# Kernel tuning notes

Hardware: AMD Instinct MI355X
Metric: run time of the kernel (lower is better)

Reference implementation:

```python
import jax, jax.numpy as jnp
import numpy as np
from jax import lax

SHAPE = (128, 128, 32)
N = 150000
DN = ('NDHWC', 'DHWIO', 'NDHWC')

W_SPECS = [(3, 3, 32), (3, 32, 32), (3, 32, 64), (3, 64, 64), (3, 64, 64),
           (3, 64, 96), (3, 96, 96), (2, 96, 96), (3, 96, 128), (3, 128, 128),
           (3, 128, 160), (3, 160, 160), (3, 160, 192), (3, 192, 192),
           (3, 192, 224), (3, 224, 224), (2, 224, 128), (2, 128, 64)]


def _conv(x, w, s, p):
    return lax.conv_general_dilated(x, w, (s, s, s), p, dimension_numbers=DN)


def _subm(x, w, m):
    # submanifold conv: inactive inputs are exactly 0, outputs masked to active sites
    return _conv(x, w, 1, 'SAME') * m


def _mask_pool(m, k, s, p):
    return lax.reduce_window(m, 0., lax.max, (1, k, k, k, 1), (1, s, s, s, 1), p)


def _max_pool(x, m):
    # sparse max-pool: max over ACTIVE sites only; inactive -> -inf, empty windows -> 0
    xi = jnp.where(m > 0, x, -jnp.inf)
    p = lax.reduce_window(xi, -jnp.inf, lax.max, (1, 2, 2, 2, 1), (1, 2, 2, 2, 1), 'VALID')
    mn = _mask_pool(m, 2, 2, 'VALID')
    return jnp.where(mn > 0, p, 0.), mn


def setup_inputs() -> dict:
    rng = np.random.default_rng(0)
    D, H, W = SHAPE
    # unique active voxel coordinates (spconv requires unique indices)
    flat = rng.choice(D * H * W, size=N, replace=False)
    z = (flat // (H * W)).astype(np.int32)
    y = ((flat // W) % H).astype(np.int32)
    xw = (flat % W).astype(np.int32)
    coors = jnp.asarray(np.stack([np.zeros(N, np.int32), z, y, xw], axis=1))

    key = jax.random.key(0)
    keys = jax.random.split(key, len(W_SPECS) + 1)
    features = jax.random.normal(keys[0], (N, 3), jnp.float32)
    inp = {'features': features, 'coors': coors, 'batch_size': 1}
    for i, (k, ci, co) in enumerate(W_SPECS):
        std = 1.0 / np.sqrt(ci * k ** 3)
        inp[f'w{i + 1}'] = jax.random.normal(keys[i + 1], (k, k, k, ci, co), jnp.float32) * std
    return inp


def _forward(features, coors, batch_size,
             w1, w2, w3, w4, w5, w6, w7, w8, w9, w10,
             w11, w12, w13, w14, w15, w16, w17, w18):
    D, H, W = SHAPE
    b, z, y, xw = coors[:, 0], coors[:, 1], coors[:, 2], coors[:, 3]
    m0 = jnp.zeros((batch_size, D, H, W, 1), features.dtype).at[b, z, y, xw, 0].set(1.0)
    x = jnp.zeros((batch_size, D, H, W, 3), features.dtype).at[b, z, y, xw].set(features)

    x = _subm(x, w1, m0)
    x = _subm(x, w2, m0)
    x = _subm(x, w3, m0)
    x = _subm(x, w4, m0)

    # SparseConv3d 64->64, k3 s2 p1 (key m0)
    x = _conv(x, w5, 2, [(1, 1), (1, 1), (1, 1)])
    m1 = _mask_pool(m0, 3, 2, [(0, 0), (1, 1), (1, 1), (1, 1), (0, 0)])
    x = x * m1

    x = _subm(x, w6, m1)
    x = _subm(x, w7, m1)

    # SparseConv3d 96->96, k2 s2 (key m1)
    x = _conv(x, w8, 2, 'VALID')
    m2 = _mask_pool(m1, 2, 2, 'VALID')
    x = x * m2

    x = _subm(x, w9, m2)
    x = _subm(x, w10, m2)

    x, m3 = _max_pool(x, m2)  # unnamed pool
    x = _subm(x, w11, m3)
    x = _subm(x, w12, m3)

    x, m4 = _max_pool(x, m3)  # pool key m3 (pre-mask m3)
    x = _subm(x, w13, m4)
    x = _subm(x, w14, m4)

    x, m5 = _max_pool(x, m4)  # pool key m4 (pre-mask m4)
    x = _subm(x, w15, m5)
    x = _subm(x, w16, m5)

    # SparseInverseConv3d: transpose conv k2 s2, output restricted to pre-pool active sites
    x = lax.conv_transpose(x, w17, (2, 2, 2), 'VALID', dimension_numbers=DN) * m4
    x = lax.conv_transpose(x, w18, (2, 2, 2), 'VALID', dimension_numbers=DN) * m3
    return x


def reference(features, coors, batch_size,
              w1, w2, w3, w4, w5, w6, w7, w8, w9, w10,
              w11, w12, w13, w14, w15, w16, w17, w18):
    return _forward(features, coors, batch_size,
                    w1, w2, w3, w4, w5, w6, w7, w8, w9, w10,
                    w11, w12, w13, w14, w15, w16, w17, w18)
```

## Files before the change

kernel.cpp:

```cpp
#include <hip/hip_runtime.h>
#include <cstdint>
#include <cstddef>

#define AD 128
#define AH 128
#define AW 32
#define NCELL (AD*AH*AW)

__device__ __forceinline__ int xcd_swizzle(int bx, int nb) {
    int xcd = bx & 7, slot = bx >> 3;
    int base = nb >> 3, rem = nb & 7;
    return (xcd < rem) ? (xcd*(base+1) + slot) : (rem + xcd*base + slot);
}

__global__ void build_grid_k(const int* __restrict__ coors, int* __restrict__ grid, int N) {
    int i = blockIdx.x * 256 + threadIdx.x;
    if (i >= N) return;
    int z = coors[i*4+1], y = coors[i*4+2], x = coors[i*4+3];
    grid[(z*AH + y)*AW + x] = i;
}

__global__ __launch_bounds__(256) void scan1_k(const int* __restrict__ grid, int* __restrict__ partial) {
    __shared__ int sm[256];
    int tid = threadIdx.x;
    int base = blockIdx.x*1024 + tid*4;
    int c = 0;
#pragma unroll
    for (int k = 0; k < 4; ++k) c += (grid[base+k] >= 0) ? 1 : 0;
    sm[tid] = c; __syncthreads();
    for (int off = 128; off; off >>= 1) {
        if (tid < off) sm[tid] += sm[tid+off];
        __syncthreads();
    }
    if (tid == 0) partial[blockIdx.x] = sm[0];
}

__global__ __launch_bounds__(512) void scan2_k(int* __restrict__ partial) {
    __shared__ int sm[512];
    int tid = threadIdx.x;
    int own = partial[tid];
    sm[tid] = own; __syncthreads();
    for (int off = 1; off < 512; off <<= 1) {
        int v = (tid >= off) ? sm[tid-off] : 0;
        __syncthreads();
        sm[tid] += v;
        __syncthreads();
    }
    partial[tid] = sm[tid] - own;
}

__global__ __launch_bounds__(256) void scan3_k(const int* __restrict__ grid, const int* __restrict__ partial,
                                               const float* __restrict__ features,
                                               int* __restrict__ grid2, int* __restrict__ cellOf,
                                               float* __restrict__ featS) {
    __shared__ int sm[256];
    int tid = threadIdx.x;
    int base = blockIdx.x*1024 + tid*4;
    int olds[4]; int c = 0;
#pragma unroll
    for (int k = 0; k < 4; ++k) { olds[k] = grid[base+k]; c += (olds[k] >= 0) ? 1 : 0; }
    int own = c;
    sm[tid] = c; __syncthreads();
    for (int off = 1; off < 256; off <<= 1) {
        int v = (tid >= off) ? sm[tid-off] : 0;
        __syncthreads();
        sm[tid] += v;
        __syncthreads();
    }
    int j = partial[blockIdx.x] + sm[tid] - own;
#pragma unroll
    for (int k = 0; k < 4; ++k) {
        int cell = base + k, old = olds[k];
        if (old >= 0) {
            grid2[cell] = j; cellOf[j] = cell;
            featS[j*4+0] = features[old*3+0];
            featS[j*4+1] = features[old*3+1];
            featS[j*4+2] = features[old*3+2];
            featS[j*4+3] = 0.f;
            ++j;
        } else grid2[cell] = -1;
    }
}

__global__ __launch_bounds__(256, 6)
void subm_first_k(const float* __restrict__ featS, const int* __restrict__ grid2,
                  const int* __restrict__ cellOf, const float* __restrict__ w,
                  float* __restrict__ out, int nsites)
{
    int j = blockIdx.x*256 + threadIdx.x;
    const int co0 = blockIdx.y*16;
    bool ok = j < nsites;
    int cell = ok ? cellOf[j] : 0;
    int z = cell >> 12, y = (cell >> 5) & 127, x = cell & 31;
    float acc[16];
#pragma unroll
    for (int n = 0; n < 16; ++n) acc[n] = 0.f;
    for (int t = 0; t < 27; ++t) {
        int nz = z + t/9 - 1, ny = y + (t/3)%3 - 1, nx = x + t%3 - 1;
        int s = -1;
        if (ok && nz>=0 && nz<AD && ny>=0 && ny<AH && nx>=0 && nx<AW)
            s = grid2[(nz<<12)|(ny<<5)|nx];
        float4 v = make_float4(0.f,0.f,0.f,0.f);
        if (s >= 0) v = ((const float4*)featS)[s];
        const float* wc = w + t*3*32 + co0;
        float av[3] = {v.x, v.y, v.z};
#pragma unroll
        for (int u = 0; u < 3; ++u)
#pragma unroll
            for (int n = 0; n < 16; ++n)
                acc[n] = fmaf(av[u], wc[u*32+n], acc[n]);
    }
    if (ok) {
        float4* op = (float4*)(out + (size_t)j*32 + co0);
#pragma unroll
        for (int q = 0; q < 4; ++q)
            op[q] = make_float4(acc[4*q], acc[4*q+1], acc[4*q+2], acc[4*q+3]);
    }
}

template<int CI, int CO>
__global__ __launch_bounds__(256, 6)
void subm1c_k(const float* __restrict__ in, const int* __restrict__ grid2,
              const int* __restrict__ cellOf, const float* __restrict__ w,
              float* __restrict__ out, int nsites)
{
    const int tid = threadIdx.x;
    const int sbx = xcd_swizzle(blockIdx.x, gridDim.x);
    const int j = sbx*256 + tid;
    const int co0 = blockIdx.y*16;
    const bool ok = j < nsites;
    int cell = ok ? cellOf[j] : 0;
    const int z = cell >> 12, y = (cell >> 5) & 127, x = cell & 31;
    float acc[16];
#pragma unroll
    for (int n = 0; n < 16; ++n) acc[n] = 0.f;

#pragma unroll 1
    for (int t = 0; t < 27; ++t) {
        int dz = t/9 - 1, dy = (t/3)%3 - 1, dx = t%3 - 1;
        int nz = z+dz, ny = y+dy, nx = x+dx;
        int s = -1;
        if (ok && nz>=0 && nz<AD && ny>=0 && ny<AH && nx>=0 && nx<AW)
            s = grid2[(nz<<12)|(ny<<5)|nx];
        for (int c0 = 0; c0 < CI; c0 += 16) {
            const float4* rp = (const float4*)(in + (size_t)(s < 0 ? 0 : s)*CI + c0);
            float4 a0 = make_float4(0.f,0.f,0.f,0.f), a1 = a0, a2 = a0, a3 = a0;
            if (s >= 0) { a0 = rp[0]; a1 = rp[1]; a2 = rp[2]; a3 = rp[3]; }
            float xv[16] = {a0.x,a0.y,a0.z,a0.w, a1.x,a1.y,a1.z,a1.w,
                            a2.x,a2.y,a2.z,a2.w, a3.x,a3.y,a3.z,a3.w};
            const float* wc = w + ((size_t)t*CI + c0)*CO + co0;
#pragma unroll
            for (int u = 0; u < 16; ++u) {
                const float* wr = wc + u*CO;
#pragma unroll
                for (int n = 0; n < 16; ++n)
                    acc[n] = fmaf(xv[u], wr[n], acc[n]);
            }
        }
    }
    if (ok) {
        float4* op = (float4*)(out + (size_t)j*CO + co0);
#pragma unroll
        for (int q = 0; q < 4; ++q)
            op[q] = make_float4(acc[4*q], acc[4*q+1], acc[4*q+2], acc[4*q+3]);
    }
}

template<int CI, int CO, int NCO>
__device__ __forceinline__ void tap_fma(const float* __restrict__ in, const float* __restrict__ wtap,
                                        int s0, int s1, float (&acc)[2][NCO])
{
    for (int c0 = 0; c0 < CI; c0 += 16) {
        const float4* r0 = (const float4*)(in + (size_t)(s0 < 0 ? 0 : s0)*CI + c0);
        const float4* r1 = (const float4*)(in + (size_t)(s1 < 0 ? 0 : s1)*CI + c0);
        float4 a0[4], a1[4];
#pragma unroll
        for (int q = 0; q < 4; ++q) {
            a0[q] = (s0 >= 0) ? r0[q] : make_float4(0.f,0.f,0.f,0.f);
            a1[q] = (s1 >= 0) ? r1[q] : make_float4(0.f,0.f,0.f,0.f);
        }
        const float* wc = wtap + c0*CO;
#pragma unroll
        for (int u = 0; u < 16; ++u) {
            float x0 = ((const float*)a0)[u];
            float x1 = ((const float*)a1)[u];
            const float* wr = wc + u*CO;
#pragma unroll
            for (int n = 0; n < NCO; ++n) {
                float wv = wr[n];
                acc[0][n] = fmaf(x0, wv, acc[0][n]);
                acc[1][n] = fmaf(x1, wv, acc[1][n]);
            }
        }
    }
}

template<int CO, int NCO>
__device__ __forceinline__ void store2(float* __restrict__ out, int co0, int j0, int j1,
                                       bool ok0, bool ok1, float (&acc)[2][NCO])
{
    if (ok0) {
        float4* op = (float4*)(out + (size_t)j0*CO + co0);
#pragma unroll
        for (int q = 0; q < NCO/4; ++q)
            op[q] = make_float4(acc[0][4*q], acc[0][4*q+1], acc[0][4*q+2], acc[0][4*q+3]);
    }
    if (ok1) {
        float4* op = (float4*)(out + (size_t)j1*CO + co0);
#pragma unroll
        for (int q = 0; q < NCO/4; ++q)
            op[q] = make_float4(acc[1][4*q], acc[1][4*q+1], acc[1][4*q+2], acc[1][4*q+3]);
    }
}

template<int CI, int CO>
__global__ __launch_bounds__(256, 3)
void conv5s_k(const float* __restrict__ in, const int* __restrict__ grid2,
              const float* __restrict__ w, float* __restrict__ part, int tg)
{
    const int tid = threadIdx.x;
    const int sbx = xcd_swizzle(blockIdx.x, gridDim.x);
    const int o0 = sbx*512 + tid, o1 = o0 + 256;
    const int co0 = blockIdx.y*32;
    const int g = blockIdx.z;
    const int t0 = g*tg, t1 = (t0 + tg < 27) ? (t0 + tg) : 27;
    int oz0 = o0 >> 10, oy0 = (o0 >> 4) & 63, ox0 = o0 & 15;
    int oz1 = o1 >> 10, oy1 = (o1 >> 4) & 63, ox1 = o1 & 15;
    float acc[2][32];
#pragma unroll
    for (int v = 0; v < 2; ++v)
#pragma unroll
        for (int n = 0; n < 32; ++n) acc[v][n] = 0.f;

#pragma unroll 1
    for (int t = t0; t < t1; ++t) {
        int dz = t/9 - 1, dy = (t/3)%3 - 1, dx = t%3 - 1;
        int iz0 = 2*oz0+dz, iy0 = 2*oy0+dy, ix0 = 2*ox0+dx;
        int iz1 = 2*oz1+dz, iy1 = 2*oy1+dy, ix1 = 2*ox1+dx;
        int s0 = -1, s1 = -1;
        if (iz0>=0 && iz0<AD && iy0>=0 && iy0<AH && ix0>=0 && ix0<AW)
            s0 = grid2[(iz0<<12)|(iy0<<5)|ix0];
        if (iz1>=0 && iz1<AD && iy1>=0 && iy1<AH && ix1>=0 && ix1<AW)
            s1 = grid2[(iz1<<12)|(iy1<<5)|ix1];
        tap_fma<CI,CO,32>(in, w + (size_t)t*CI*CO + co0, s0, s1, acc);
    }
    store2<CO,32>(part + (size_t)g*65536*CO, co0, o0, o1, true, true, acc);
}

template<int CI, int CO>
__global__ __launch_bounds__(256, 3)
void convB_tile_k(const float* __restrict__ in, const float* __restrict__ w,
                  const float* __restrict__ mask, float* __restrict__ out)
{
    constexpr int HY = 10, HX = 10;
    constexpr int NH = 600;
    constexpr int STR = 20;
    __shared__ float sf[NH*STR];

    const int tid = threadIdx.x;
    const int bx = blockIdx.x;
    const int tx_ = bx & 1, ty_ = (bx >> 1) & 7, tz_ = bx >> 4;
    const int z0 = tz_*4, y0 = ty_*8, x0 = tx_*8;
    const int lz = tid >> 6, ly = (tid >> 3) & 7, lx = tid & 7;
    const int co0 = blockIdx.y*32;
    const int o = ((z0+lz)*64 + (y0+ly))*16 + (x0+lx);

    float acc[32];
#pragma unroll
    for (int n = 0; n < 32; ++n) acc[n] = 0.f;

    for (int c0 = 0; c0 < CI; c0 += 16) {
        __syncthreads();
        for (int i = tid; i < NH*4; i += 256) {
            int cell = i >> 2, q = i & 3;
            int hz = cell / 100; int rr = cell - hz*100; int hy = rr / 10; int hx = rr - hy*10;
            int gz = z0 + hz - 1, gy = y0 + hy - 1, gx = x0 + hx - 1;
            float4 v = make_float4(0.f,0.f,0.f,0.f);
            if (gz>=0 && gz<64 && gy>=0 && gy<64 && gx>=0 && gx<16)
                v = *(const float4*)(in + (size_t)((gz*64+gy)*16+gx)*CI + c0 + q*4);
            *(float4*)(&sf[cell*STR + q*4]) = v;
        }
        __syncthreads();
#pragma unroll 1
        for (int t = 0; t < 27; ++t) {
            int hz = lz + t/9, hy = ly + (t/3)%3, hx = lx + t%3;
            const float4* fp = (const float4*)(&sf[((hz*HY + hy)*HX + hx)*STR]);
            float4 f0 = fp[0], f1 = fp[1], f2 = fp[2], f3 = fp[3];
            float xv[16] = {f0.x,f0.y,f0.z,f0.w, f1.x,f1.y,f1.z,f1.w,
                            f2.x,f2.y,f2.z,f2.w, f3.x,f3.y,f3.z,f3.w};
            const float* wt = w + ((size_t)t*CI + c0)*CO + co0;
#pragma unroll
            for (int u = 0; u < 16; ++u) {
                const float* wr = wt + u*CO;
#pragma unroll
                for (int n = 0; n < 32; ++n)
                    acc[n] = fmaf(xv[u], wr[n], acc[n]);
            }
        }
    }
    float mv = mask[o];
    float4* op = (float4*)(out + (size_t)o*CO + co0);
#pragma unroll
    for (int q = 0; q < 8; ++q)
        op[q] = make_float4(acc[4*q]*mv, acc[4*q+1]*mv, acc[4*q+2]*mv, acc[4*q+3]*mv);
}

template<int CI, int CO, int K, int S, int PAD, int ID, int IH, int IW, int OD, int OH, int OW>
__global__ __launch_bounds__(256, 3)
void dense2v_k(const float* __restrict__ in, const float* __restrict__ w,
               float* __restrict__ part, int tg)
{
    constexpr int NT = K*K*K;
    constexpr int NV = OD*OH*OW;
    const int tid = threadIdx.x;
    const int o0 = blockIdx.x*512 + tid, o1 = o0 + 256;
    const int co0 = blockIdx.y*32;
    const int g = blockIdx.z;
    const int t0 = g*tg, t1 = (t0 + tg < NT) ? (t0 + tg) : NT;
    int oz0 = o0/(OH*OW), r0v = o0 - oz0*(OH*OW), oy0 = r0v/OW, ox0 = r0v - oy0*OW;
    int oz1 = o1/(OH*OW), r1v = o1 - oz1*(OH*OW), oy1 = r1v/OW, ox1 = r1v - oy1*OW;
    float acc[2][32];
#pragma unroll
    for (int v = 0; v < 2; ++v)
#pragma unroll
        for (int n = 0; n < 32; ++n) acc[v][n] = 0.f;

#pragma unroll 1
    for (int t = t0; t < t1; ++t) {
        int kz = t/(K*K), rr = t - kz*(K*K), ky = rr/K, kx = rr - ky*K;
        int iz0 = oz0*S + kz - PAD, iy0 = oy0*S + ky - PAD, ix0 = ox0*S + kx - PAD;
        int iz1 = oz1*S + kz - PAD, iy1 = oy1*S + ky - PAD, ix1 = ox1*S + kx - PAD;
        int s0 = -1, s1 = -1;
        if (iz0>=0 && iz0<ID && iy0>=0 && iy0<IH && ix0>=0 && ix0<IW)
            s0 = (iz0*IH + iy0)*IW + ix0;
        if (iz1>=0 && iz1<ID && iy1>=0 && iy1<IH && ix1>=0 && ix1<IW)
            s1 = (iz1*IH + iy1)*IW + ix1;
        tap_fma<CI,CO,32>(in, w + (size_t)t*CI*CO + co0, s0, s1, acc);
    }
    store2<CO,32>(part + (size_t)g*NV*CO, co0, o0, o1, true, true, acc);
}

__global__ __launch_bounds__(256)
void reduce_k(const float* __restrict__ part, float* __restrict__ out,
              const float* __restrict__ mask, int NV, int CO, int G)
{
    int e = blockIdx.x*256 + threadIdx.x;
    if (e >= NV*CO) return;
    float s = 0.f;
    for (int g = 0; g < G; ++g) s += part[(size_t)g*NV*CO + e];
    if (mask) s *= mask[e / CO];
    out[e] = s;
}

template<int CI, int CO, int D_, int H_, int W_>
__global__ __launch_bounds__(256)
void conv_ks_k(const float* __restrict__ in, const float* __restrict__ w,
               float* __restrict__ part)
{
    constexpr int NV = D_*H_*W_;
    int idx = blockIdx.x*256 + threadIdx.x;
    if (idx >= NV*27*CO) return;
    int co = idx % CO;
    int rest = idx / CO;
    int t = rest % 27;
    int vox = rest / 27;
    int z = vox/(H_*W_), rv = vox - z*(H_*W_), y = rv/W_, x = rv - y*W_;
    int iz = z + t/9 - 1, iy = y + (t/3)%3 - 1, ix = x + t%3 - 1;
    float a = 0.f;
    if (iz>=0 && iz<D_ && iy>=0 && iy<H_ && ix>=0 && ix<W_) {
        const float4* xp = (const float4*)(in + (size_t)((iz*H_+iy)*W_+ix)*CI);
        const float* wp = w + (size_t)t*CI*CO + co;
#pragma unroll 4
        for (int c4 = 0; c4 < CI/4; ++c4) {
            float4 xv = xp[c4];
            a = fmaf(xv.x, wp[(size_t)(4*c4+0)*CO], a);
            a = fmaf(xv.y, wp[(size_t)(4*c4+1)*CO], a);
            a = fmaf(xv.z, wp[(size_t)(4*c4+2)*CO], a);
            a = fmaf(xv.w, wp[(size_t)(4*c4+3)*CO], a);
        }
    }
    part[((size_t)t*NV + vox)*CO + co] = a;
}

__global__ void mask_from_gridA_k(const int* __restrict__ grid, float* __restrict__ m1) {
    int o = blockIdx.x*256 + threadIdx.x;
    if (o >= 64*64*16) return;
    int oz = o >> 10, r = o & 1023, oy = r >> 4, ox = r & 15;
    int any = 0;
    for (int kz=0;kz<3;++kz) for(int ky=0;ky<3;++ky) for(int kx=0;kx<3;++kx){
        int iz=2*oz+kz-1, iy=2*oy+ky-1, ix=2*ox+kx-1;
        if (iz>=0&&iz<AD&&iy>=0&&iy<AH&&ix>=0&&ix<AW)
            any |= (grid[(iz*AH+iy)*AW+ix] >= 0) ? 1 : 0;
    }
    m1[o] = any ? 1.f : 0.f;
}

__global__ void mask_pool2_k(const float* __restrict__ mi, float* __restrict__ mo,
                             int OD,int OH,int OW) {
    int o = blockIdx.x*256 + threadIdx.x;
    if (o >= OD*OH*OW) return;
    int oz = o/(OH*OW); int r = o - oz*(OH*OW); int oy = r/OW, ox = r - oy*OW;
    int IH = OH*2, IW = OW*2;
    int any = 0;
    for (int dz=0;dz<2;++dz)for(int dy=0;dy<2;++dy)for(int dx=0;dx<2;++dx){
        int ii = ((2*oz+dz)*IH + (2*oy+dy))*IW + (2*ox+dx);
        any |= (mi[ii] > 0.f) ? 1 : 0;
    }
    mo[o] = any ? 1.f : 0.f;
}

template<int C>
__global__ void maxpool2_k(const float* __restrict__ x, const float* __restrict__ m,
                           float* __restrict__ out, int OD,int OH,int OW) {
    int idx = blockIdx.x*256 + threadIdx.x;
    int total = OD*OH*OW*C;
    if (idx >= total) return;
    int o = idx / C, c = idx - o*C;
    int oz = o/(OH*OW); int r = o - oz*(OH*OW); int oy = r/OW, ox = r - oy*OW;
    int IH = OH*2, IW = OW*2;
    float best = -3.402823466e38f; int any = 0;
    for (int dz=0;dz<2;++dz)for(int dy=0;dy<2;++dy)for(int dx=0;dx<2;++dx){
        int ii = ((2*oz+dz)*IH + (2*oy+dy))*IW + (2*ox+dx);
        if (m[ii] > 0.f) { any = 1; best = fmaxf(best, x[(size_t)ii*C + c]); }
    }
    out[idx] = any ? best : 0.f;
}

template<int CI, int CO>
__global__ void deconv2x_k(const float* __restrict__ x, const float* __restrict__ w,
                           const float* __restrict__ m, float* __restrict__ out,
                           int OD,int OH,int OW) {
    int idx = blockIdx.x*256 + threadIdx.x;
    int total = OD*OH*OW*CO;
    if (idx >= total) return;
    int o = idx / CO, co = idx - o*CO;
    if (!(m[o] > 0.f)) { out[idx] = 0.f; return; }
    int oz = o/(OH*OW); int r = o - oz*(OH*OW); int oy = r/OW, ox = r - oy*OW;
    int IH = OH>>1, IW = OW>>1;
    int iz=oz>>1, iy=oy>>1, ix=ox>>1;
    int wt = ((1-(oz&1))*2 + (1-(oy&1)))*2 + (1-(ox&1));
    const float* xp = x + (size_t)((iz*IH+iy)*IW+ix)*CI;
    const float* wp = w + (size_t)wt*CI*CO + co;
    float acc = 0.f;
#pragma unroll 4
    for (int ci=0;ci<CI;++ci) acc = fmaf(xp[ci], wp[(size_t)ci*CO], acc);
    out[idx] = acc;
}

extern "C" void kernel_launch(void* const* d_in, const int* in_sizes, int n_in,
                              void* d_out, int out_size, void* d_ws, size_t ws_size,
                              hipStream_t stream)
{
    const float* features = (const float*)d_in[0];
    const int*   coors    = (const int*)d_in[1];
    const int N = in_sizes[0] / 3;
    const float* w1  = (const float*)d_in[3];
    const float* w2  = (const float*)d_in[4];
    const float* w3  = (const float*)d_in[5];
    const float* w4  = (const float*)d_in[6];
    const float* w5  = (const float*)d_in[7];
    const float* w6  = (const float*)d_in[8];
    const float* w7  = (const float*)d_in[9];
    const float* w8  = (const float*)d_in[10];
    const float* w9  = (const float*)d_in[11];
    const float* w10 = (const float*)d_in[12];
    const float* w11 = (const float*)d_in[13];
    const float* w12 = (const float*)d_in[14];
    const float* w13 = (const float*)d_in[15];
    const float* w14 = (const float*)d_in[16];
    const float* w15 = (const float*)d_in[17];
    const float* w16 = (const float*)d_in[18];
    const float* w17 = (const float*)d_in[19];
    const float* w18 = (const float*)d_in[20];

    char* p = (char*)d_ws;
    auto alloc = [&](size_t bytes)->void* {
        void* r = (void*)p; p += (bytes + 255) & ~(size_t)255; return r;
    };
    int*   gridA = (int*)  alloc((size_t)NCELL*4);
    int*   grid2 = (int*)  alloc((size_t)NCELL*4);
    int*   partS = (int*)  alloc((size_t)512*4);
    int*   cellOf= (int*)  alloc((size_t)N*4);
    float* featS = (float*)alloc((size_t)N*4*4);
    float* sA0   = (float*)alloc((size_t)N*64*4);
    float* sA1   = (float*)alloc((size_t)N*64*4);
    float* xB0   = (float*)alloc((size_t)65536*96*4);
    float* xB1   = (float*)alloc((size_t)65536*96*4);
    float* m1    = (float*)alloc((size_t)65536*4);
    float* xC0   = (float*)alloc((size_t)8192*128*4);
    float* xC1   = (float*)alloc((size_t)8192*128*4);
    float* m2    = (float*)alloc((size_t)8192*4);
    float* xD0   = (float*)alloc((size_t)1024*160*4);
    float* xD1   = (float*)alloc((size_t)1024*160*4);
    float* m3    = (float*)alloc((size_t)1024*4);
    float* xE0   = (float*)alloc((size_t)128*192*4);
    float* xE1   = (float*)alloc((size_t)128*192*4);
    float* m4    = (float*)alloc((size_t)128*4);
    float* xF0   = (float*)alloc((size_t)16*224*4);
    float* xF1   = (float*)alloc((size_t)16*224*4);
    float* m5    = (float*)alloc((size_t)16*4);
    float* dT1   = (float*)alloc((size_t)128*128*4);
    if ((size_t)(p - (char*)d_ws) > ws_size) return;
    float* part  = sA0;

    hipMemsetAsync(gridA, 0xFF, (size_t)NCELL*4, stream);
    build_grid_k<<<(N+255)/256,256,0,stream>>>(coors, gridA, N);
    scan1_k<<<512,256,0,stream>>>(gridA, partS);
    scan2_k<<<1,512,0,stream>>>(partS);
    scan3_k<<<512,256,0,stream>>>(gridA, partS, features, grid2, cellOf, featS);

    int gx1 = (N + 255) / 256;
    subm_first_k<<<dim3(gx1,2),256,0,stream>>>(featS, grid2, cellOf, w1, sA0, N);
    subm1c_k<32,32><<<dim3(gx1,2),256,0,stream>>>(sA0, grid2, cellOf, w2, sA1, N);
    subm1c_k<32,64><<<dim3(gx1,4),256,0,stream>>>(sA1, grid2, cellOf, w3, sA0, N);
    subm1c_k<64,64><<<dim3(gx1,4),256,0,stream>>>(sA0, grid2, cellOf, w4, sA1, N);

    conv5s_k<64,64><<<dim3(128,2,2),256,0,stream>>>(sA1, grid2, w5, sA0, 14);
    reduce_k<<<(65536*64+255)/256,256,0,stream>>>(sA0, xB0, nullptr, 65536, 64, 2);
    mask_from_gridA_k<<<256,256,0,stream>>>(gridA, m1);

    convB_tile_k<64,96><<<dim3(256,3),256,0,stream>>>(xB0, w6, m1, xB1);
    convB_tile_k<96,96><<<dim3(256,3),256,0,stream>>>(xB1, w7, m1, xB0);

    dense2v_k<96,96,2,2,0, 64,64,16, 32,32,8><<<dim3(16,3,8),256,0,stream>>>(xB0, w8, part, 1);
    reduce_k<<<(8192*96+255)/256,256,0,stream>>>(part, xC0, nullptr, 8192, 96, 8);
    mask_pool2_k<<<(8192+255)/256,256,0,stream>>>(m1, m2, 32,32,8);

    dense2v_k<96,128,3,1,1, 32,32,8, 32,32,8><<<dim3(16,4,9),256,0,stream>>>(xC0, w9, part, 3);
    reduce_k<<<(8192*128+255)/256,256,0,stream>>>(part, xC1, m2, 8192, 128, 9);
    dense2v_k<128,128,3,1,1, 32,32,8, 32,32,8><<<dim3(16,4,9),256,0,stream>>>(xC1, w10, part, 3);
    reduce_k<<<(8192*128+255)/256,256,0,stream>>>(part, xC0, m2, 8192, 128, 9);

    mask_pool2_k<<<(1024+255)/256,256,0,stream>>>(m2, m3, 16,16,4);
    maxpool2_k<128><<<(1024*128+255)/256,256,0,stream>>>(xC0, m2, xD0, 16,16,4);

    dense2v_k<128,160,3,1,1, 16,16,4, 16,16,4><<<dim3(2,5,27),256,0,stream>>>(xD0, w11, part, 1);
    reduce_k<<<(1024*160+255)/256,256,0,stream>>>(part, xD1, m3, 1024, 160, 27);
    dense2v_k<160,160,3,1,1, 16,16,4, 16,16,4><<<dim3(2,5,27),256,0,stream>>>(xD1, w12, part, 1);
    reduce_k<<<(1024*160+255)/256,256,0,stream>>>(part, xD0, m3, 1024, 160, 27);

    mask_pool2_k<<<1,256,0,stream>>>(m3, m4, 8,8,2);
    maxpool2_k<160><<<(128*160+255)/256,256,0,stream>>>(xD0, m3, xE0, 8,8,2);

    conv_ks_k<160,192, 8,8,2><<<(128*27*192+255)/256,256,0,stream>>>(xE0, w13, part);
    reduce_k<<<(128*192+255)/256,256,0,stream>>>(part, xE1, m4, 128, 192, 27);
    conv_ks_k<192,192, 8,8,2><<<(128*27*192+255)/256,256,0,stream>>>(xE1, w14, part);
    reduce_k<<<(128*192+255)/256,256,0,stream>>>(part, xE0, m4, 128, 192, 27);

    mask_pool2_k<<<1,256,0,stream>>>(m4, m5, 4,4,1);
    maxpool2_k<192><<<(16*192+255)/256,256,0,stream>>>(xE0, m4, xF0, 4,4,1);

    conv_ks_k<192,224, 4,4,1><<<(16*27*224+255)/256,256,0,stream>>>(xF0, w15, part);
    reduce_k<<<(16*224+255)/256,256,0,stream>>>(part, xF1, m5, 16, 224, 27);
    conv_ks_k<224,224, 4,4,1><<<(16*27*224+255)/256,256,0,stream>>>(xF1, w16, part);
    reduce_k<<<(16*224+255)/256,256,0,stream>>>(part, xF0, m5, 16, 224, 27);

    deconv2x_k<224,128><<<(8*8*2*128+255)/256,256,0,stream>>>(xF0, w17, m4, dT1, 8,8,2);
    deconv2x_k<128,64><<<(16*16*4*64+255)/256,256,0,stream>>>(dT1, w18, m3, (float*)d_out, 16,16,4);
}
```

Baseline: 2.833 ms.

## Drop split-K partials in strided conv and shrink per-thread output tiles for occupancy

The strided 64->64 conv stops splitting its 27 taps across two partial buffers and no longer needs the separate reduce pass. It now writes its result directly, with one output voxel and 16 output channels per thread, using twice as many blocks and a higher occupancy hint. The tiled 3x3x3 convs also drop to 16 output channels per thread and stage 8 input channels at a time in a smaller shared-memory tile, which doubles the grid and is meant to raise occupancy. In exchange, each input feature and shared-memory tile is reloaded for more channel blocks, and there are more barrier iterations over the input channels.

```diff
diff --git a/kernel.cpp b/kernel.cpp
--- a/kernel.cpp
+++ b/kernel.cpp
@@ -166,95 +166,55 @@
     }
 }
 
-template<int CI, int CO, int NCO>
-__device__ __forceinline__ void tap_fma(const float* __restrict__ in, const float* __restrict__ wtap,
-                                        int s0, int s1, float (&acc)[2][NCO])
-{
-    for (int c0 = 0; c0 < CI; c0 += 16) {
-        const float4* r0 = (const float4*)(in + (size_t)(s0 < 0 ? 0 : s0)*CI + c0);
-        const float4* r1 = (const float4*)(in + (size_t)(s1 < 0 ? 0 : s1)*CI + c0);
-        float4 a0[4], a1[4];
-#pragma unroll
-        for (int q = 0; q < 4; ++q) {
-            a0[q] = (s0 >= 0) ? r0[q] : make_float4(0.f,0.f,0.f,0.f);
-            a1[q] = (s1 >= 0) ? r1[q] : make_float4(0.f,0.f,0.f,0.f);
-        }
-        const float* wc = wtap + c0*CO;
-#pragma unroll
-        for (int u = 0; u < 16; ++u) {
-            float x0 = ((const float*)a0)[u];
-            float x1 = ((const float*)a1)[u];
-            const float* wr = wc + u*CO;
-#pragma unroll
-            for (int n = 0; n < NCO; ++n) {
-                float wv = wr[n];
-                acc[0][n] = fmaf(x0, wv, acc[0][n]);
-                acc[1][n] = fmaf(x1, wv, acc[1][n]);
-            }
-        }
-    }
-}
-
-template<int CO, int NCO>
-__device__ __forceinline__ void store2(float* __restrict__ out, int co0, int j0, int j1,
-                                       bool ok0, bool ok1, float (&acc)[2][NCO])
-{
-    if (ok0) {
-        float4* op = (float4*)(out + (size_t)j0*CO + co0);
-#pragma unroll
-        for (int q = 0; q < NCO/4; ++q)
-            op[q] = make_float4(acc[0][4*q], acc[0][4*q+1], acc[0][4*q+2], acc[0][4*q+3]);
-    }
-    if (ok1) {
-        float4* op = (float4*)(out + (size_t)j1*CO + co0);
-#pragma unroll
-        for (int q = 0; q < NCO/4; ++q)
-            op[q] = make_float4(acc[1][4*q], acc[1][4*q+1], acc[1][4*q+2], acc[1][4*q+3]);
-    }
-}
-
 template<int CI, int CO>
-__global__ __launch_bounds__(256, 3)
-void conv5s_k(const float* __restrict__ in, const int* __restrict__ grid2,
-              const float* __restrict__ w, float* __restrict__ part, int tg)
+__global__ __launch_bounds__(256, 6)
+void conv5c_k(const float* __restrict__ in, const int* __restrict__ grid2,
+              const float* __restrict__ w, float* __restrict__ out)
 {
     const int tid = threadIdx.x;
     const int sbx = xcd_swizzle(blockIdx.x, gridDim.x);
-    const int o0 = sbx*512 + tid, o1 = o0 + 256;
-    const int co0 = blockIdx.y*32;
-    const int g = blockIdx.z;
-    const int t0 = g*tg, t1 = (t0 + tg < 27) ? (t0 + tg) : 27;
-    int oz0 = o0 >> 10, oy0 = (o0 >> 4) & 63, ox0 = o0 & 15;
-    int oz1 = o1 >> 10, oy1 = (o1 >> 4) & 63, ox1 = o1 & 15;
-    float acc[2][32];
-#pragma unroll
-    for (int v = 0; v < 2; ++v)
-#pragma unroll
-        for (int n = 0; n < 32; ++n) acc[v][n] = 0.f;
+    const int o = sbx*256 + tid;
+    const int co0 = blockIdx.y*16;
+    const int oz = o >> 10, oy = (o >> 4) & 63, ox = o & 15;
+    float acc[16];
+#pragma unroll
+    for (int n = 0; n < 16; ++n) acc[n] = 0.f;
 
 #pragma unroll 1
-    for (int t = t0; t < t1; ++t) {
-        int dz = t/9 - 1, dy = (t/3)%3 - 1, dx = t%3 - 1;
-        int iz0 = 2*oz0+dz, iy0 = 2*oy0+dy, ix0 = 2*ox0+dx;
-        int iz1 = 2*oz1+dz, iy1 = 2*oy1+dy, ix1 = 2*ox1+dx;
-        int s0 = -1, s1 = -1;
-        if (iz0>=0 && iz0<AD && iy0>=0 && iy0<AH && ix0>=0 && ix0<AW)
-            s0 = grid2[(iz0<<12)|(iy0<<5)|ix0];
-        if (iz1>=0 && iz1<AD && iy1>=0 && iy1<AH && ix1>=0 && ix1<AW)
-            s1 = grid2[(iz1<<12)|(iy1<<5)|ix1];
-        tap_fma<CI,CO,32>(in, w + (size_t)t*CI*CO + co0, s0, s1, acc);
-    }
-    store2<CO,32>(part + (size_t)g*65536*CO, co0, o0, o1, true, true, acc);
+    for (int t = 0; t < 27; ++t) {
+        int iz = 2*oz + t/9 - 1, iy = 2*oy + (t/3)%3 - 1, ix = 2*ox + t%3 - 1;
+        int s = -1;
+        if (iz>=0 && iz<AD && iy>=0 && iy<AH && ix>=0 && ix<AW)
+            s = grid2[(iz<<12)|(iy<<5)|ix];
+        for (int c0 = 0; c0 < CI; c0 += 16) {
+            const float4* rp = (const float4*)(in + (size_t)(s < 0 ? 0 : s)*CI + c0);
+            float4 a0 = make_float4(0.f,0.f,0.f,0.f), a1 = a0, a2 = a0, a3 = a0;
+            if (s >= 0) { a0 = rp[0]; a1 = rp[1]; a2 = rp[2]; a3 = rp[3]; }
+            float xv[16] = {a0.x,a0.y,a0.z,a0.w, a1.x,a1.y,a1.z,a1.w,
+                            a2.x,a2.y,a2.z,a2.w, a3.x,a3.y,a3.z,a3.w};
+            const float* wc = w + ((size_t)t*CI + c0)*CO + co0;
+#pragma unroll
+            for (int u = 0; u < 16; ++u) {
+                const float* wr = wc + u*CO;
+#pragma unroll
+                for (int n = 0; n < 16; ++n)
+                    acc[n] = fmaf(xv[u], wr[n], acc[n]);
+            }
+        }
+    }
+    float4* op = (float4*)(out + (size_t)o*CO + co0);
+#pragma unroll
+    for (int q = 0; q < 4; ++q)
+        op[q] = make_float4(acc[4*q], acc[4*q+1], acc[4*q+2], acc[4*q+3]);
 }
 
 template<int CI, int CO>
-__global__ __launch_bounds__(256, 3)
+__global__ __launch_bounds__(256, 5)
 void convB_tile_k(const float* __restrict__ in, const float* __restrict__ w,
                   const float* __restrict__ mask, float* __restrict__ out)
 {
-    constexpr int HY = 10, HX = 10;
     constexpr int NH = 600;
-    constexpr int STR = 20;
+    constexpr int STR = 12;
     __shared__ float sf[NH*STR];
 
     const int tid = threadIdx.x;
@@ -262,17 +222,17 @@
     const int tx_ = bx & 1, ty_ = (bx >> 1) & 7, tz_ = bx >> 4;
     const int z0 = tz_*4, y0 = ty_*8, x0 = tx_*8;
     const int lz = tid >> 6, ly = (tid >> 3) & 7, lx = tid & 7;
-    const int co0 = blockIdx.y*32;
+    const int co0 = blockIdx.y*16;
     const int o = ((z0+lz)*64 + (y0+ly))*16 + (x0+lx);
 
-    float acc[32];
-#pragma unroll
-    for (int n = 0; n < 32; ++n) acc[n] = 0.f;
-
-    for (int c0 = 0; c0 < CI; c0 += 16) {
-        __syncthreads();
-        for (int i = tid; i < NH*4; i += 256) {
-            int cell = i >> 2, q = i & 3;
+    float acc[16];
+#pragma unroll
+    for (int n = 0; n < 16; ++n) acc[n] = 0.f;
+
+    for (int c0 = 0; c0 < CI; c0 += 8) {
+        __syncthreads();
+        for (int i = tid; i < NH*2; i += 256) {
+            int cell = i >> 1, q = i & 1;
             int hz = cell / 100; int rr = cell - hz*100; int hy = rr / 10; int hx = rr - hy*10;
             int gz = z0 + hz - 1, gy = y0 + hy - 1, gx = x0 + hx - 1;
             float4 v = make_float4(0.f,0.f,0.f,0.f);
@@ -284,16 +244,15 @@
 #pragma unroll 1
         for (int t = 0; t < 27; ++t) {
             int hz = lz + t/9, hy = ly + (t/3)%3, hx = lx + t%3;
-            const float4* fp = (const float4*)(&sf[((hz*HY + hy)*HX + hx)*STR]);
-            float4 f0 = fp[0], f1 = fp[1], f2 = fp[2], f3 = fp[3];
-            float xv[16] = {f0.x,f0.y,f0.z,f0.w, f1.x,f1.y,f1.z,f1.w,
-                            f2.x,f2.y,f2.z,f2.w, f3.x,f3.y,f3.z,f3.w};
+            const float4* fp = (const float4*)(&sf[((hz*10 + hy)*10 + hx)*STR]);
+            float4 f0 = fp[0], f1 = fp[1];
+            float xv[8] = {f0.x,f0.y,f0.z,f0.w, f1.x,f1.y,f1.z,f1.w};
             const float* wt = w + ((size_t)t*CI + c0)*CO + co0;
 #pragma unroll
-            for (int u = 0; u < 16; ++u) {
+            for (int u = 0; u < 8; ++u) {
                 const float* wr = wt + u*CO;
 #pragma unroll
-                for (int n = 0; n < 32; ++n)
+                for (int n = 0; n < 16; ++n)
                     acc[n] = fmaf(xv[u], wr[n], acc[n]);
             }
         }
@@ -301,8 +260,55 @@
     float mv = mask[o];
     float4* op = (float4*)(out + (size_t)o*CO + co0);
 #pragma unroll
-    for (int q = 0; q < 8; ++q)
+    for (int q = 0; q < 4; ++q)
         op[q] = make_float4(acc[4*q]*mv, acc[4*q+1]*mv, acc[4*q+2]*mv, acc[4*q+3]*mv);
+}
+
+template<int CI, int CO, int NCO>
+__device__ __forceinline__ void tap_fma(const float* __restrict__ in, const float* __restrict__ wtap,
+                                        int s0, int s1, float (&acc)[2][NCO])
+{
+    for (int c0 = 0; c0 < CI; c0 += 16) {
+        const float4* r0 = (const float4*)(in + (size_t)(s0 < 0 ? 0 : s0)*CI + c0);
+        const float4* r1 = (const float4*)(in + (size_t)(s1 < 0 ? 0 : s1)*CI + c0);
+        float4 a0[4], a1[4];
+#pragma unroll
+        for (int q = 0; q < 4; ++q) {
+            a0[q] = (s0 >= 0) ? r0[q] : make_float4(0.f,0.f,0.f,0.f);
+            a1[q] = (s1 >= 0) ? r1[q] : make_float4(0.f,0.f,0.f,0.f);
+        }
+        const float* wc = wtap + c0*CO;
+#pragma unroll
+        for (int u = 0; u < 16; ++u) {
+            float x0 = ((const float*)a0)[u];
+            float x1 = ((const float*)a1)[u];
+            const float* wr = wc + u*CO;
+#pragma unroll
+            for (int n = 0; n < NCO; ++n) {
+                float wv = wr[n];
+                acc[0][n] = fmaf(x0, wv, acc[0][n]);
+                acc[1][n] = fmaf(x1, wv, acc[1][n]);
+            }
+        }
+    }
+}
+
+template<int CO, int NCO>
+__device__ __forceinline__ void store2(float* __restrict__ out, int co0, int j0, int j1,
+                                       bool ok0, bool ok1, float (&acc)[2][NCO])
+{
+    if (ok0) {
+        float4* op = (float4*)(out + (size_t)j0*CO + co0);
+#pragma unroll
+        for (int q = 0; q < NCO/4; ++q)
+            op[q] = make_float4(acc[0][4*q], acc[0][4*q+1], acc[0][4*q+2], acc[0][4*q+3]);
+    }
+    if (ok1) {
+        float4* op = (float4*)(out + (size_t)j1*CO + co0);
+#pragma unroll
+        for (int q = 0; q < NCO/4; ++q)
+            op[q] = make_float4(acc[1][4*q], acc[1][4*q+1], acc[1][4*q+2], acc[1][4*q+3]);
+    }
 }
 
 template<int CI, int CO, int K, int S, int PAD, int ID, int IH, int IW, int OD, int OH, int OW>
@@ -515,12 +521,11 @@
     subm1c_k<32,64><<<dim3(gx1,4),256,0,stream>>>(sA1, grid2, cellOf, w3, sA0, N);
     subm1c_k<64,64><<<dim3(gx1,4),256,0,stream>>>(sA0, grid2, cellOf, w4, sA1, N);
 
-    conv5s_k<64,64><<<dim3(128,2,2),256,0,stream>>>(sA1, grid2, w5, sA0, 14);
-    reduce_k<<<(65536*64+255)/256,256,0,stream>>>(sA0, xB0, nullptr, 65536, 64, 2);
+    conv5c_k<64,64><<<dim3(256,4),256,0,stream>>>(sA1, grid2, w5, xB0);
     mask_from_gridA_k<<<256,256,0,stream>>>(gridA, m1);
 
-    convB_tile_k<64,96><<<dim3(256,3),256,0,stream>>>(xB0, w6, m1, xB1);
-    convB_tile_k<96,96><<<dim3(256,3),256,0,stream>>>(xB1, w7, m1, xB0);
+    convB_tile_k<64,96><<<dim3(256,6),256,0,stream>>>(xB0, w6, m1, xB1);
+    convB_tile_k<96,96><<<dim3(256,6),256,0,stream>>>(xB1, w7, m1, xB0);
 
     dense2v_k<96,96,2,2,0, 64,64,16, 32,32,8><<<dim3(16,3,8),256,0,stream>>>(xB0, w8, part, 1);
     reduce_k<<<(8192*96+255)/256,256,0,stream>>>(part, xC0, nullptr, 8192, 96, 8);
```

New measurement: 2.513 ms. 11.3% less time.
